# Performance work log

Measured on AMD Instinct MI355X. Metric: run time of the kernel, lower is better.

The kernel has to match this reference:

```python
import jax, jax.numpy as jnp
from jax import lax
import numpy as np

NUM_HEADS = 8
PATCH = 16
EPS_SUM = 1e-6


def resize_nearest(x, H, W):
    # torch F.interpolate(mode='nearest'): src = floor(dst * in / out)
    ih, iw = x.shape[-2], x.shape[-1]
    ri = (jnp.arange(H) * ih) // H
    ci = (jnp.arange(W) * iw) // W
    return x[:, :, ri][:, :, :, ci]


def single_scale(x, delta, wq, bq, ws, bs):
    # x: [1+K, C, H, W]; delta: [K, 1, H0, W0]
    q, s = x[:1], x[1:]
    K, C, H, W = s.shape
    d = C // NUM_HEADS
    P = PATCH
    Hp, Wp = H // P, W // P
    S = P * P
    delta = resize_nearest(delta, H, W)  # [K,1,H,W]

    qf = jnp.transpose(q, (0, 2, 3, 1))[0] @ wq.T + bq            # [H,W,C]
    qh = qf.reshape(H, W, NUM_HEADS, d).transpose(2, 0, 1, 3)     # [h,H,W,d]
    sf = jnp.transpose(s, (0, 2, 3, 1)) @ ws.T + bs               # [K,H,W,C]
    sh = sf.reshape(K, H, W, NUM_HEADS, d).transpose(0, 3, 1, 2, 4)  # [K,h,H,W,d]

    fg = delta.reshape(K, P, Hp, P, Wp).transpose(0, 1, 3, 2, 4).reshape(K, S, Hp * Wp)
    bg = 1.0 - fg
    fg_sum = jnp.maximum(fg.sum(-1), EPS_SUM)  # [K,S]
    bg_sum = jnp.maximum(bg.sum(-1), EPS_SUM)

    sp = sh.reshape(K, NUM_HEADS, P, Hp, P, Wp, d).transpose(0, 1, 2, 4, 3, 5, 6)
    sp = sp.reshape(K, NUM_HEADS, S, Hp * Wp, d)  # [K,h,S,l,d]

    c_fg = jnp.einsum('ksl,khsld->khsd', fg, sp) / fg_sum[:, None, :, None]
    c_bg = jnp.einsum('ksl,khsld->khsd', bg, sp) / bg_sum[:, None, :, None]
    # concat along prototype dim then flatten as [h, K*2S, d] (K-major, fg-then-bg)
    c_s = jnp.concatenate([c_fg, c_bg], axis=2).transpose(1, 0, 2, 3).reshape(NUM_HEADS, K * 2 * S, d)
    v = jnp.concatenate([jnp.ones((K, S), c_s.dtype), jnp.zeros((K, S), c_s.dtype)], axis=1).reshape(-1)  # [K*2S]

    mask = jnp.concatenate([
        jnp.where(fg_sum < 1.0, -jnp.inf, 0.0),
        jnp.where(bg_sum < 1.0, -jnp.inf, 0.0)], axis=1).reshape(-1)  # [K*2S]

    attn = jnp.einsum('hyxd,hsd->hyxs', qh, c_s) + mask  # [h,H,W,K*2S]
    attn = jax.nn.softmax(attn, axis=-1)
    out = jnp.einsum('hyxs,s->hyx', attn, v)  # [h,H,W]
    return out.mean(0)[None, None]  # [1,1,H,W]


def group_norm(x, gamma, beta, groups=4, eps=1e-5):
    N, C, H, W = x.shape
    xr = x.reshape(N, groups, C // groups, H, W)
    mu = xr.mean((2, 3, 4), keepdims=True)
    var = xr.var((2, 3, 4), keepdims=True)
    xr = (xr - mu) * lax.rsqrt(var + eps)
    return xr.reshape(N, C, H, W) * gamma[None, :, None, None] + beta[None, :, None, None]


def conv2d(x, w, b, pad):
    y = lax.conv_general_dilated(x, w, (1, 1), [(pad, pad), (pad, pad)],
                                 dimension_numbers=('NCHW', 'OIHW', 'NCHW'))
    return y + b[None, :, None, None]


def setup_inputs() -> dict:
    key = jax.random.key(0)
    ks = jax.random.split(key, 24)
    K, C, H, W = 5, 256, 64, 64
    inp = {}
    for i in range(4):
        inp[f'x{i}'] = jax.random.normal(ks[i], (1 + K, C, H, W), jnp.float32)
    inp['delta_onehot_x'] = jax.random.randint(ks[4], (K, 1, 256, 256), 0, 2).astype(jnp.float32)
    inp['wq'] = jax.random.normal(ks[5], (C, C), jnp.float32) * 0.02
    inp['bq'] = jnp.zeros((C,), jnp.float32)
    inp['ws'] = jax.random.normal(ks[6], (C, C), jnp.float32) * 0.02
    inp['bs'] = jnp.zeros((C,), jnp.float32)
    inp['cw1'] = jax.random.normal(ks[7], (16, 4, 5, 5), jnp.float32) * 0.05
    inp['cb1'] = jnp.zeros((16,), jnp.float32)
    inp['g1'] = jnp.ones((16,), jnp.float32)
    inp['be1'] = jnp.zeros((16,), jnp.float32)
    inp['cw2'] = jax.random.normal(ks[8], (64, 16, 5, 5), jnp.float32) * 0.05
    inp['cb2'] = jnp.zeros((64,), jnp.float32)
    inp['g2'] = jnp.ones((64,), jnp.float32)
    inp['be2'] = jnp.zeros((64,), jnp.float32)
    inp['cw3'] = jax.random.normal(ks[9], (128, 64, 3, 3), jnp.float32) * 0.05
    inp['cb3'] = jnp.zeros((128,), jnp.float32)
    inp['g3'] = jnp.ones((128,), jnp.float32)
    inp['be3'] = jnp.zeros((128,), jnp.float32)
    return inp


def reference(x0, x1, x2, x3, delta_onehot_x, wq, bq, ws, bs,
              cw1, cb1, g1, be1, cw2, cb2, g2, be2, cw3, cb3, g3, be3):
    masks = [single_scale(x, delta_onehot_x, wq, bq, ws, bs) for x in (x0, x1, x2, x3)]
    cm = jnp.concatenate(masks, axis=1)  # [1, nlayers=4, H, W]
    # idx=1 conv head: kernels [5,5,3], channels [16,64,128], GroupNorm(4)+ReLU
    h = jax.nn.relu(group_norm(conv2d(cm, cw1, cb1, 2), g1, be1))
    h = jax.nn.relu(group_norm(conv2d(h, cw2, cb2, 2), g2, be2))
    h = jax.nn.relu(group_norm(conv2d(h, cw3, cb3, 1), g3, be3))
    return h
```

## Files before the change

kernel.cpp:

```cpp
#include <hip/hip_runtime.h>
#include <hip/hip_bf16.h>
#include <stdint.h>

#define CCH 256
#define NPIX 4096
#define NH 8
#define M2 2560
#define LOG2E 1.44269504088896f
#define GN_NB 32

typedef __attribute__((ext_vector_type(8))) short short8;
typedef __attribute__((ext_vector_type(4))) float f32x4;

__device__ __forceinline__ uint16_t f2bfu(float f) {
    uint32_t u = __builtin_bit_cast(uint32_t, f);
    return (uint16_t)((u + 0x7FFFu + ((u >> 16) & 1u)) >> 16);
}
__device__ __forceinline__ uint32_t pack_bf2(float a, float b) {
    return (uint32_t)f2bfu(a) | ((uint32_t)f2bfu(b) << 16);
}
__device__ __forceinline__ short8 u4_to_s8(uint4 v) {
    return __builtin_bit_cast(short8, v);
}

__global__ void prep_wb(const float* __restrict__ wq, const float* __restrict__ wsm,
                        uint16_t* __restrict__ WB) {
    int idx = blockIdx.x * 256 + threadIdx.x;
    const float* src = (idx < 65536) ? wq : wsm;
    WB[idx] = f2bfu(src[idx & 65535]);
}

__global__ __launch_bounds__(256) void patch_sum(
        const float* __restrict__ x0, const float* __restrict__ x1,
        const float* __restrict__ x2, const float* __restrict__ x3,
        const float* __restrict__ dox, uint16_t* __restrict__ PS,
        float* __restrict__ inv, float* __restrict__ mbias) {
    int z = blockIdx.z;
    int sc = z / 5, k = z % 5;
    const float* xim = ((sc == 0) ? x0 : (sc == 1) ? x1 : (sc == 2) ? x2 : x3)
                       + (size_t)(k + 1) * CCH * NPIX;
    int p1 = blockIdx.x, chq = blockIdx.y;
    int tid = threadIdx.x;
    int cloc = tid >> 6, col = tid & 63;
    __shared__ float wls[4][64];
    __shared__ uint16_t pst[2][16][72];
    wls[cloc][col] = dox[(size_t)k * 65536 + (size_t)(16 * p1 + 4 * cloc) * 256 + 4 * col];
    __syncthreads();
    float w0 = wls[0][col], w1 = wls[1][col], w2 = wls[2][col], w3 = wls[3][col];
    const float* xbase = xim + p1 * 256 + col;
#pragma unroll 4
    for (int it = 0; it < 16; ++it) {
        int c = chq * 64 + it * 4 + cloc;
        const float* xp = xbase + (size_t)c * NPIX;
        float v0 = xp[0], v1 = xp[64], v2 = xp[128], v3 = xp[192];
        float pf = w0 * v0 + w1 * v1 + w2 * v2 + w3 * v3;
        float pb = (v0 + v1 + v2 + v3) - pf;
        pf += __shfl_xor(pf, 1); pf += __shfl_xor(pf, 2);
        pb += __shfl_xor(pb, 1); pb += __shfl_xor(pb, 2);
        if ((col & 3) == 0) {
            int q = col >> 2, cl = it * 4 + cloc;
            pst[0][q][cl] = f2bfu(pf);
            pst[1][q][cl] = f2bfu(pb);
        }
    }
    if (chq == 0 && tid < 64) {
        float ws = w0 + w1 + w2 + w3;
        ws += __shfl_xor(ws, 1); ws += __shfl_xor(ws, 2);
        if ((col & 3) == 0) {
            int s = p1 * 16 + (col >> 2);
            float fsum = ws, bsum = 16.f - ws;
            int mf = k * 512 + s, mbk = mf + 256;
            mbias[sc * M2 + mf]  = (fsum < 1.f) ? -1e30f : 0.f;
            mbias[sc * M2 + mbk] = (bsum < 1.f) ? -1e30f : 0.f;
            inv[(size_t)(z * 2 + 0) * 256 + s] = 1.f / fmaxf(fsum, 1e-6f);
            inv[(size_t)(z * 2 + 1) * 256 + s] = 1.f / fmaxf(bsum, 1e-6f);
        }
    }
    __syncthreads();
    int fb = tid >> 7, rem = tid & 127;
    int q = rem >> 3, chunk = rem & 7;
    uint4 v = *(const uint4*)&pst[fb][q][chunk * 8];
    int s = p1 * 16 + q;
    *(uint4*)&PS[((size_t)(z * 2 + fb) * 256 + s) * CCH + chq * 64 + chunk * 8] = v;
}

__global__ __launch_bounds__(256) void cent_gemm(
        const uint16_t* __restrict__ PS, const uint16_t* __restrict__ WB,
        const float* __restrict__ bs, const float* __restrict__ inv,
        uint16_t* __restrict__ Csbf) {
    int tid = threadIdx.x, lane = tid & 63, wid = tid >> 6;
    int lp = lane & 15, g = lane >> 4;
    int rowb = blockIdx.x * 128 + wid * 32;
    int cob = blockIdx.y * 64;
    const uint16_t* wsb = WB + 65536;
    f32x4 acc[2][4] = {};
#pragma unroll
    for (int ks = 0; ks < 8; ++ks) {
        int k0 = ks * 32;
        uint4 a0 = *(const uint4*)(PS + (size_t)(rowb + lp) * CCH + k0 + g * 8);
        uint4 a1 = *(const uint4*)(PS + (size_t)(rowb + 16 + lp) * CCH + k0 + g * 8);
        short8 af[2] = {u4_to_s8(a0), u4_to_s8(a1)};
        short8 b[4];
#pragma unroll
        for (int t = 0; t < 4; ++t) {
            uint4 bw = *(const uint4*)(wsb + (size_t)(cob + t * 16 + lp) * 256 + k0 + g * 8);
            b[t] = u4_to_s8(bw);
        }
#pragma unroll
        for (int m = 0; m < 2; ++m)
#pragma unroll
            for (int t = 0; t < 4; ++t)
                acc[m][t] = __builtin_amdgcn_mfma_f32_16x16x32_bf16(af[m], b[t], acc[m][t], 0, 0, 0);
    }
#pragma unroll
    for (int m = 0; m < 2; ++m)
#pragma unroll
        for (int t = 0; t < 4; ++t) {
            int co = cob + t * 16 + lp;
            int h = co >> 5, d = co & 31;
            float bv = bs[co];
#pragma unroll
            for (int r = 0; r < 4; ++r) {
                int row = rowb + m * 16 + g * 4 + r;
                int zz = row >> 9, fb = (row >> 8) & 1, s = row & 255;
                int scc = zz / 5, kk = zz % 5;
                int slot = kk * 512 + fb * 256 + s;
                float val = acc[m][t][r] * inv[row] + bv;
                Csbf[(((size_t)scc * NH + h) * M2 + slot) * 32 + d] = f2bfu(val);
            }
        }
}

__global__ __launch_bounds__(512) void q_gemm(
        const float* __restrict__ x0, const float* __restrict__ x1,
        const float* __restrict__ x2, const float* __restrict__ x3,
        const uint16_t* __restrict__ WB, const float* __restrict__ bq,
        uint16_t* __restrict__ Qbf) {
    int sc = blockIdx.y;
    const float* xim = (sc == 0) ? x0 : (sc == 1) ? x1 : (sc == 2) ? x2 : x3;
    int p0 = blockIdx.x * 64;
    int tid = threadIdx.x, lane = tid & 63, wid = tid >> 6;
    int lp = lane & 15, g = lane >> 4;
    int wm = wid >> 1, wn = wid & 1;
    __shared__ uint32_t Al[16][68];
    f32x4 acc[8] = {};
#pragma unroll
    for (int ks = 0; ks < 8; ++ks) {
        int k0 = ks * 32;
        __syncthreads();
        if (tid < 256) {
            int rp = tid >> 4, f4i = tid & 15;
            float4 v0 = *(const float4*)(xim + (size_t)(k0 + 2 * rp) * NPIX + p0 + f4i * 4);
            float4 v1 = *(const float4*)(xim + (size_t)(k0 + 2 * rp + 1) * NPIX + p0 + f4i * 4);
            *(uint4*)&Al[rp][f4i * 4] = make_uint4(
                pack_bf2(v0.x, v1.x), pack_bf2(v0.y, v1.y),
                pack_bf2(v0.z, v1.z), pack_bf2(v0.w, v1.w));
        }
        __syncthreads();
        short8 b[8];
#pragma unroll
        for (int tn = 0; tn < 8; ++tn) {
            uint4 bw = *(const uint4*)(WB + (size_t)(wn * 128 + tn * 16 + lp) * 256 + k0 + g * 8);
            b[tn] = u4_to_s8(bw);
        }
        int px = wm * 16 + lp;
        uint4 av = make_uint4(Al[4 * g + 0][px], Al[4 * g + 1][px],
                              Al[4 * g + 2][px], Al[4 * g + 3][px]);
        short8 af = u4_to_s8(av);
#pragma unroll
        for (int tn = 0; tn < 8; ++tn)
            acc[tn] = __builtin_amdgcn_mfma_f32_16x16x32_bf16(af, b[tn], acc[tn], 0, 0, 0);
    }
#pragma unroll
    for (int tn = 0; tn < 8; ++tn) {
        int co = wn * 128 + tn * 16 + lp;
        float bv = bq[co];
#pragma unroll
        for (int r = 0; r < 4; ++r) {
            int row = p0 + wm * 16 + g * 4 + r;
            Qbf[((size_t)(sc * NPIX + row)) * CCH + co] = f2bfu((acc[tn][r] + bv) * LOG2E);
        }
    }
}

__global__ __launch_bounds__(256) void attn_v3(
        const uint16_t* __restrict__ Qbf, const uint16_t* __restrict__ Csbf,
        const float* __restrict__ mbias, float* __restrict__ sfbuf) {
    int head = blockIdx.y;
    int sc = blockIdx.z >> 2, split = blockIdx.z & 3;
    int tid = threadIdx.x;
    int lane = tid & 63, wid = tid >> 6;
    int lp = lane & 15, g = lane >> 4;
    int p0w = blockIdx.x * 128 + wid * 32;

    const uint16_t* Qs = Qbf + (size_t)sc * NPIX * CCH;
    const uint16_t* csb = Csbf + ((size_t)sc * NH + head) * M2 * 32;
    const float* mb = mbias + sc * M2;

    uint4 qv0 = *(const uint4*)(Qs + (size_t)(p0w + lp) * CCH + head * 32 + g * 8);
    uint4 qv1 = *(const uint4*)(Qs + (size_t)(p0w + 16 + lp) * CCH + head * 32 + g * 8);
    short8 aq[2] = {u4_to_s8(qv0), u4_to_s8(qv1)};

    float s[2][4] = {}, f[2][4] = {};
    int cbeg = split * 640;
#pragma unroll 2
    for (int c0loc = 0; c0loc < 640; c0loc += 64) {
        int c0 = cbeg + c0loc;
        bool fg = ((c0 & 511) < 256);
        short8 bf[4];
        float mbv[4];
#pragma unroll
        for (int t = 0; t < 4; t++) {
            int row = c0 + t * 16 + lp;
            uint4 bw = *(const uint4*)(csb + (size_t)row * 32 + g * 8);
            bf[t] = u4_to_s8(bw);
            mbv[t] = mb[row];
        }
        float se[2][4] = {};
#pragma unroll
        for (int m = 0; m < 2; m++)
#pragma unroll
            for (int t = 0; t < 4; t++) {
                f32x4 c = {mbv[t], mbv[t], mbv[t], mbv[t]};
                c = __builtin_amdgcn_mfma_f32_16x16x32_bf16(aq[m], bf[t], c, 0, 0, 0);
#pragma unroll
                for (int r = 0; r < 4; r++)
                    se[m][r] += __builtin_amdgcn_exp2f(c[r]);
            }
#pragma unroll
        for (int m = 0; m < 2; m++)
#pragma unroll
            for (int r = 0; r < 4; r++)
                s[m][r] += se[m][r];
        if (fg) {
#pragma unroll
            for (int m = 0; m < 2; m++)
#pragma unroll
                for (int r = 0; r < 4; r++)
                    f[m][r] += se[m][r];
        }
    }
#pragma unroll
    for (int m = 0; m < 2; m++)
#pragma unroll
        for (int r = 0; r < 4; r++) {
#pragma unroll
            for (int msk = 1; msk < 16; msk <<= 1) {
                s[m][r] += __shfl_xor(s[m][r], msk);
                f[m][r] += __shfl_xor(f[m][r], msk);
            }
        }
    if (lp == 0) {
        float* sf = sfbuf + (size_t)((sc * 4 + split) * 2) * NH * NPIX;
        float* so = sf + (size_t)head * NPIX;
        float* fo = sf + (size_t)(NH + head) * NPIX;
#pragma unroll
        for (int m = 0; m < 2; m++)
#pragma unroll
            for (int r = 0; r < 4; r++) {
                int px = p0w + m * 16 + g * 4 + r;
                so[px] = s[m][r];
                fo[px] = f[m][r];
            }
    }
}

__global__ void mean_heads3(const float* __restrict__ sfbuf, float* __restrict__ cm) {
    int idx = blockIdx.x * 256 + threadIdx.x;
    int sc = idx >> 12, p = idx & 4095;
    const float* b = sfbuf + (size_t)sc * 4 * 2 * NH * NPIX;
    float acc = 0.f;
#pragma unroll
    for (int h = 0; h < NH; h++) {
        float sv = 0.f, fv = 0.f;
#pragma unroll
        for (int sp = 0; sp < 4; sp++) {
            sv += b[((size_t)(sp * 2) * NH + h) * NPIX + p];
            fv += b[((size_t)(sp * 2 + 1) * NH + h) * NPIX + p];
        }
        acc += fv / sv;
    }
    cm[idx] = 0.125f * acc;
}

__global__ void prep_w(const float* __restrict__ w, uint16_t* __restrict__ Wk,
                       int Cin, int Cout, int K2, int CK) {
    int idx = blockIdx.x * 256 + threadIdx.x;
    int total = CK * Cout * 32;
    if (idx >= total) return;
    int kk = idx & 31;
    int oc = (idx >> 5) % Cout;
    int ck = idx / (32 * Cout);
    int k = ck * 32 + kk;
    int tap = k / Cin, ic = k % Cin;
    float v = (tap < K2) ? w[((size_t)oc * Cin + ic) * K2 + tap] : 0.0f;
    Wk[idx] = f2bfu(v);
}

template<int CIN, int COUT, int KSZ>
__global__ __launch_bounds__(256) void conv_mfma(
        const float* __restrict__ in, const uint16_t* __restrict__ Wk,
        const float* __restrict__ bias, float* __restrict__ out) {
    constexpr int PAD = KSZ / 2;
    constexpr int NTAP = KSZ * KSZ;
    constexpr int K = CIN * NTAP;
    constexpr int CK = (K + 31) / 32;
    constexpr int PXP = 64 + 2 * PAD;
    constexpr int ICB = (CIN >= 8) ? CIN / 8 : 1;
    __shared__ uint16_t Xs[KSZ * PXP * CIN];
    int tid = threadIdx.x;
    int lane = tid & 63, wv = tid >> 6;
    int lp = lane & 15, g = lane >> 4;
    int y = blockIdx.x;
    int oc0 = blockIdx.y * 64;

    if (CIN >= 8) {
        for (int idx = tid; idx < KSZ * ICB * PXP; idx += 256) {
            int pxp = idx % PXP; int rem = idx / PXP;
            int icb = rem % ICB; int r = rem / ICB;
            int gy = y + r - PAD, gx = pxp - PAD;
            bool ok = ((unsigned)gy < 64u) && ((unsigned)gx < 64u);
            const float* ip = in + (size_t)(icb * 8) * NPIX + gy * 64 + gx;
            uint32_t wb[4];
#pragma unroll
            for (int j = 0; j < 4; j++) {
                float v0 = ok ? ip[(size_t)(2 * j) * NPIX] : 0.f;
                float v1 = ok ? ip[(size_t)(2 * j + 1) * NPIX] : 0.f;
                wb[j] = pack_bf2(v0, v1);
            }
            *(uint4*)&Xs[(size_t)idx * 8] = make_uint4(wb[0], wb[1], wb[2], wb[3]);
        }
    } else {
        for (int idx = tid; idx < KSZ * PXP; idx += 256) {
            int pxp = idx % PXP; int r = idx / PXP;
            int gy = y + r - PAD, gx = pxp - PAD;
            bool ok = ((unsigned)gy < 64u) && ((unsigned)gx < 64u);
            const float* ip = in + (size_t)gy * 64 + gx;
            float v0 = ok ? ip[0] : 0.f, v1 = ok ? ip[NPIX] : 0.f;
            float v2 = ok ? ip[2 * NPIX] : 0.f, v3 = ok ? ip[3 * NPIX] : 0.f;
            *(uint2*)&Xs[(size_t)idx * 4] = make_uint2(pack_bf2(v0, v1), pack_bf2(v2, v3));
        }
    }
    __syncthreads();

    int tmb, tme, tn;
    if (COUT >= 64) { tn = wv; tmb = 0; tme = 4; }
    else            { tn = 0;  tmb = wv; tme = wv + 1; }
    int oc = oc0 + tn * 16 + lp;
    f32x4 acc[4] = {};

#pragma unroll
    for (int ck = 0; ck < CK; ck++) {
        const uint16_t* wp = Wk + ((size_t)ck * COUT + oc) * 32 + g * 8;
        uint4 bw = *(const uint4*)wp;
        short8 bfr = u4_to_s8(bw);
        if (CIN >= 8) {
            int gk = ck * 4 + g;
            int tap = gk / ICB; if (tap > NTAP - 1) tap = NTAP - 1;
            int icb = gk % ICB;
            int r = tap / KSZ, dx = tap % KSZ;
            int base = (r * ICB + icb) * PXP * 8;
            for (int tm = tmb; tm < tme; tm++) {
                int pxp = tm * 16 + lp + dx;
                uint4 av = *(const uint4*)&Xs[base + pxp * 8];
                short8 afr = u4_to_s8(av);
                acc[tm] = __builtin_amdgcn_mfma_f32_16x16x32_bf16(afr, bfr, acc[tm], 0, 0, 0);
            }
        } else {
            int gk = ck * 4 + g;
            int t0 = 2 * gk;     if (t0 > NTAP - 1) t0 = NTAP - 1;
            int t1 = 2 * gk + 1; if (t1 > NTAP - 1) t1 = NTAP - 1;
            int r0 = t0 / KSZ, dx0 = t0 % KSZ;
            int r1 = t1 / KSZ, dx1 = t1 % KSZ;
            for (int tm = tmb; tm < tme; tm++) {
                uint2 a0 = *(const uint2*)&Xs[((size_t)(r0 * PXP + tm * 16 + lp + dx0)) * 4];
                uint2 a1 = *(const uint2*)&Xs[((size_t)(r1 * PXP + tm * 16 + lp + dx1)) * 4];
                uint4 av = make_uint4(a0.x, a0.y, a1.x, a1.y);
                short8 afr = u4_to_s8(av);
                acc[tm] = __builtin_amdgcn_mfma_f32_16x16x32_bf16(afr, bfr, acc[tm], 0, 0, 0);
            }
        }
    }
    float bv = bias[oc];
    for (int tm = tmb; tm < tme; tm++)
#pragma unroll
        for (int r = 0; r < 4; r++) {
            int px = tm * 16 + g * 4 + r;
            out[(size_t)oc * NPIX + y * 64 + px] = acc[tm][r] + bv;
        }
}

__global__ __launch_bounds__(256) void gn_part(const float* __restrict__ in, int Cg,
                                               float* __restrict__ part) {
    int g = blockIdx.x, b = blockIdx.y;
    int n4 = Cg * 1024;
    const float4* base = (const float4*)(in + (size_t)g * Cg * NPIX);
    float s = 0.0f, s2 = 0.0f;
    for (int i = b * 256 + threadIdx.x; i < n4; i += GN_NB * 256) {
        float4 v = base[i];
        s += v.x + v.y + v.z + v.w;
        s2 = fmaf(v.x, v.x, s2); s2 = fmaf(v.y, v.y, s2);
        s2 = fmaf(v.z, v.z, s2); s2 = fmaf(v.w, v.w, s2);
    }
#pragma unroll
    for (int off = 32; off; off >>= 1) {
        s += __shfl_down(s, off);
        s2 += __shfl_down(s2, off);
    }
    __shared__ float rs[4], rs2[4];
    int w = threadIdx.x >> 6;
    if ((threadIdx.x & 63) == 0) { rs[w] = s; rs2[w] = s2; }
    __syncthreads();
    if (threadIdx.x == 0) {
        part[(g * GN_NB + b) * 2]     = rs[0] + rs[1] + rs[2] + rs[3];
        part[(g * GN_NB + b) * 2 + 1] = rs2[0] + rs2[1] + rs2[2] + rs2[3];
    }
}

__global__ __launch_bounds__(256) void gn_apply_relu(const float* __restrict__ in, const float* __restrict__ part,
                                                     const float* __restrict__ gamma, const float* __restrict__ beta,
                                                     int Cg, float* __restrict__ out) {
    int idx4 = blockIdx.x * 256 + threadIdx.x;
    int c = idx4 >> 10;
    int g = c / Cg;
    float s = 0.0f, s2 = 0.0f;
#pragma unroll
    for (int b = 0; b < GN_NB; b++) {
        s  += part[(g * GN_NB + b) * 2];
        s2 += part[(g * GN_NB + b) * 2 + 1];
    }
    float n = (float)(Cg * NPIX);
    float mu = s / n;
    float rstd = rsqrtf(s2 / n - mu * mu + 1e-5f);
    float ga = gamma[c] * rstd;
    float be = beta[c] - mu * ga;
    float4 v = ((const float4*)in)[idx4];
    float4 o;
    o.x = fmaf(v.x, ga, be); o.x = o.x > 0.f ? o.x : 0.f;
    o.y = fmaf(v.y, ga, be); o.y = o.y > 0.f ? o.y : 0.f;
    o.z = fmaf(v.z, ga, be); o.z = o.z > 0.f ? o.z : 0.f;
    o.w = fmaf(v.w, ga, be); o.w = o.w > 0.f ? o.w : 0.f;
    ((float4*)out)[idx4] = o;
}

extern "C" void kernel_launch(void* const* d_in, const int* in_sizes, int n_in,
                              void* d_out, int out_size, void* d_ws, size_t ws_size,
                              hipStream_t stream) {
    const float* x0 = (const float*)d_in[0];
    const float* x1 = (const float*)d_in[1];
    const float* x2 = (const float*)d_in[2];
    const float* x3 = (const float*)d_in[3];
    const float* dox = (const float*)d_in[4];
    const float* wq  = (const float*)d_in[5];
    const float* bq  = (const float*)d_in[6];
    const float* wsm = (const float*)d_in[7];
    const float* bs  = (const float*)d_in[8];
    const float* cw1 = (const float*)d_in[9];
    const float* cb1 = (const float*)d_in[10];
    const float* g1  = (const float*)d_in[11];
    const float* be1 = (const float*)d_in[12];
    const float* cw2 = (const float*)d_in[13];
    const float* cb2 = (const float*)d_in[14];
    const float* g2  = (const float*)d_in[15];
    const float* be2 = (const float*)d_in[16];
    const float* cw3 = (const float*)d_in[17];
    const float* cb3 = (const float*)d_in[18];
    const float* g3  = (const float*)d_in[19];
    const float* be3 = (const float*)d_in[20];

    uint16_t* Qbf  = (uint16_t*)d_ws;
    uint16_t* Csbf = Qbf + (size_t)4194304;
    uint16_t* PS   = Csbf + (size_t)2621440;
    uint16_t* WB   = PS + (size_t)2621440;
    uint16_t* Wk1  = WB + 131072;
    uint16_t* Wk2  = Wk1 + 2048;
    uint16_t* Wk3  = Wk2 + 26624;
    float* fbase  = (float*)(Wk3 + 73728);
    float* mbias  = fbase;
    float* inv    = mbias + 10240;
    float* sfbuf  = inv + 10240;
    float* cm     = sfbuf + 1048576;
    float* h1     = cm + 16384;
    float* h2     = h1 + 65536;
    float* h3     = h2 + 262144;
    float* gnpart = h3 + 524288;

    prep_wb<<<512, 256, 0, stream>>>(wq, wsm, WB);
    prep_w<<<(4 * 16 * 32 + 255) / 256, 256, 0, stream>>>(cw1, Wk1, 4, 16, 25, 4);
    prep_w<<<(13 * 64 * 32 + 255) / 256, 256, 0, stream>>>(cw2, Wk2, 16, 64, 25, 13);
    prep_w<<<(18 * 128 * 32 + 255) / 256, 256, 0, stream>>>(cw3, Wk3, 64, 128, 9, 18);

    patch_sum<<<dim3(16, 4, 20), 256, 0, stream>>>(x0, x1, x2, x3, dox, PS, inv, mbias);
    q_gemm<<<dim3(64, 4), 512, 0, stream>>>(x0, x1, x2, x3, WB, bq, Qbf);
    cent_gemm<<<dim3(80, 4), 256, 0, stream>>>(PS, WB, bs, inv, Csbf);
    attn_v3<<<dim3(32, NH, 16), 256, 0, stream>>>(Qbf, Csbf, mbias, sfbuf);
    mean_heads3<<<64, 256, 0, stream>>>(sfbuf, cm);

    conv_mfma<4, 16, 5><<<dim3(64, 1), 256, 0, stream>>>(cm, Wk1, cb1, h1);
    gn_part<<<dim3(4, GN_NB), 256, 0, stream>>>(h1, 4, gnpart);
    gn_apply_relu<<<(16 * 1024) / 256, 256, 0, stream>>>(h1, gnpart, g1, be1, 4, h1);

    conv_mfma<16, 64, 5><<<dim3(64, 1), 256, 0, stream>>>(h1, Wk2, cb2, h2);
    gn_part<<<dim3(4, GN_NB), 256, 0, stream>>>(h2, 16, gnpart);
    gn_apply_relu<<<(64 * 1024) / 256, 256, 0, stream>>>(h2, gnpart, g2, be2, 16, h2);

    conv_mfma<64, 128, 3><<<dim3(64, 2), 256, 0, stream>>>(h2, Wk3, cb3, h3);
    gn_part<<<dim3(4, GN_NB), 256, 0, stream>>>(h3, 32, gnpart);
    gn_apply_relu<<<(128 * 1024) / 256, 256, 0, stream>>>(h3, gnpart, g3, be3, 32, (float*)d_out);
}
```

Measured before the change: 156.4 us.

## Double pixels per wave in attention and split fg/bg accumulators

Result: faster. 151.7 us (-3.0%).

```diff
diff --git a/kernel.cpp b/kernel.cpp
--- a/kernel.cpp
+++ b/kernel.cpp
@@ -183,7 +183,7 @@
     }
 }
 
-__global__ __launch_bounds__(256) void attn_v3(
+__global__ __launch_bounds__(256) void attn_v4(
         const uint16_t* __restrict__ Qbf, const uint16_t* __restrict__ Csbf,
         const float* __restrict__ mbias, float* __restrict__ sfbuf) {
     int head = blockIdx.y;
@@ -191,19 +191,21 @@
     int tid = threadIdx.x;
     int lane = tid & 63, wid = tid >> 6;
     int lp = lane & 15, g = lane >> 4;
-    int p0w = blockIdx.x * 128 + wid * 32;
+    int p0w = blockIdx.x * 256 + wid * 64;
 
     const uint16_t* Qs = Qbf + (size_t)sc * NPIX * CCH;
     const uint16_t* csb = Csbf + ((size_t)sc * NH + head) * M2 * 32;
     const float* mb = mbias + sc * M2;
 
-    uint4 qv0 = *(const uint4*)(Qs + (size_t)(p0w + lp) * CCH + head * 32 + g * 8);
-    uint4 qv1 = *(const uint4*)(Qs + (size_t)(p0w + 16 + lp) * CCH + head * 32 + g * 8);
-    short8 aq[2] = {u4_to_s8(qv0), u4_to_s8(qv1)};
-
-    float s[2][4] = {}, f[2][4] = {};
+    short8 aq[4];
+#pragma unroll
+    for (int m = 0; m < 4; m++) {
+        uint4 qv = *(const uint4*)(Qs + (size_t)(p0w + m * 16 + lp) * CCH + head * 32 + g * 8);
+        aq[m] = u4_to_s8(qv);
+    }
+
+    float sfg[4][4] = {}, sbg[4][4] = {};
     int cbeg = split * 640;
-#pragma unroll 2
     for (int c0loc = 0; c0loc < 640; c0loc += 64) {
         int c0 = cbeg + c0loc;
         bool fg = ((c0 & 511) < 256);
@@ -216,38 +218,38 @@
             bf[t] = u4_to_s8(bw);
             mbv[t] = mb[row];
         }
-        float se[2][4] = {};
-#pragma unroll
-        for (int m = 0; m < 2; m++)
-#pragma unroll
-            for (int t = 0; t < 4; t++) {
-                f32x4 c = {mbv[t], mbv[t], mbv[t], mbv[t]};
-                c = __builtin_amdgcn_mfma_f32_16x16x32_bf16(aq[m], bf[t], c, 0, 0, 0);
-#pragma unroll
-                for (int r = 0; r < 4; r++)
-                    se[m][r] += __builtin_amdgcn_exp2f(c[r]);
-            }
-#pragma unroll
-        for (int m = 0; m < 2; m++)
-#pragma unroll
-            for (int r = 0; r < 4; r++)
-                s[m][r] += se[m][r];
         if (fg) {
 #pragma unroll
-            for (int m = 0; m < 2; m++)
-#pragma unroll
-                for (int r = 0; r < 4; r++)
-                    f[m][r] += se[m][r];
-        }
-    }
-#pragma unroll
-    for (int m = 0; m < 2; m++)
+            for (int m = 0; m < 4; m++)
+#pragma unroll
+                for (int t = 0; t < 4; t++) {
+                    f32x4 c = {mbv[t], mbv[t], mbv[t], mbv[t]};
+                    c = __builtin_amdgcn_mfma_f32_16x16x32_bf16(aq[m], bf[t], c, 0, 0, 0);
+#pragma unroll
+                    for (int r = 0; r < 4; r++)
+                        sfg[m][r] += __builtin_amdgcn_exp2f(c[r]);
+                }
+        } else {
+#pragma unroll
+            for (int m = 0; m < 4; m++)
+#pragma unroll
+                for (int t = 0; t < 4; t++) {
+                    f32x4 c = {mbv[t], mbv[t], mbv[t], mbv[t]};
+                    c = __builtin_amdgcn_mfma_f32_16x16x32_bf16(aq[m], bf[t], c, 0, 0, 0);
+#pragma unroll
+                    for (int r = 0; r < 4; r++)
+                        sbg[m][r] += __builtin_amdgcn_exp2f(c[r]);
+                }
+        }
+    }
+#pragma unroll
+    for (int m = 0; m < 4; m++)
 #pragma unroll
         for (int r = 0; r < 4; r++) {
 #pragma unroll
             for (int msk = 1; msk < 16; msk <<= 1) {
-                s[m][r] += __shfl_xor(s[m][r], msk);
-                f[m][r] += __shfl_xor(f[m][r], msk);
+                sfg[m][r] += __shfl_xor(sfg[m][r], msk);
+                sbg[m][r] += __shfl_xor(sbg[m][r], msk);
             }
         }
     if (lp == 0) {
@@ -255,12 +257,12 @@
         float* so = sf + (size_t)head * NPIX;
         float* fo = sf + (size_t)(NH + head) * NPIX;
 #pragma unroll
-        for (int m = 0; m < 2; m++)
+        for (int m = 0; m < 4; m++)
 #pragma unroll
             for (int r = 0; r < 4; r++) {
                 int px = p0w + m * 16 + g * 4 + r;
-                so[px] = s[m][r];
-                fo[px] = f[m][r];
+                so[px] = sfg[m][r] + sbg[m][r];
+                fo[px] = sfg[m][r];
             }
     }
 }
@@ -493,7 +495,7 @@
     patch_sum<<<dim3(16, 4, 20), 256, 0, stream>>>(x0, x1, x2, x3, dox, PS, inv, mbias);
     q_gemm<<<dim3(64, 4), 512, 0, stream>>>(x0, x1, x2, x3, WB, bq, Qbf);
     cent_gemm<<<dim3(80, 4), 256, 0, stream>>>(PS, WB, bs, inv, Csbf);
-    attn_v3<<<dim3(32, NH, 16), 256, 0, stream>>>(Qbf, Csbf, mbias, sfbuf);
+    attn_v4<<<dim3(16, NH, 16), 256, 0, stream>>>(Qbf, Csbf, mbias, sfbuf);
     mean_heads3<<<64, 256, 0, stream>>>(sfbuf, cm);
 
     conv_mfma<4, 16, 5><<<dim3(64, 1), 256, 0, stream>>>(cm, Wk1, cb1, h1);
```
